# Optimization experiments

Hardware: AMD Instinct MI355X
Metric: run time of the kernel (lower is better)

Reference implementation:

```python
import jax, jax.numpy as jnp
import numpy as np

B, T, HID = 2, 2048, 2048
NH = 8
D = HID // NH  # head_dim = 256 (expand_ratio=1 so input_dim == hidden_size)
EPS_RMS = 1e-8   # RMSNorm inside BitLinear
EPS_LN = 1e-5    # layernorm_eps for g_norm


def _rms(x, w, eps):
    # weighted RMSNorm over last dim
    return x * jax.lax.rsqrt(jnp.mean(x * x, axis=-1, keepdims=True) + eps) * w


def _act_quant(x):
    # per-token 8-bit fake quant with straight-through estimator
    s = 127.0 / jnp.clip(jnp.max(jnp.abs(x), axis=-1, keepdims=True), 1e-5)
    q = jnp.clip(jnp.round(x * s), -128, 127) / s
    return x + jax.lax.stop_gradient(q - x)


def _weight_quant(w):
    # ternary weight quantization (BitNet b1.58) with STE
    s = 1.0 / jnp.clip(jnp.mean(jnp.abs(w)), 1e-5)
    q = jnp.clip(jnp.round(w * s), -1, 1) / s
    return w + jax.lax.stop_gradient(q - w)


def _bitlinear(x, w, norm_w):
    # FusedBitLinear: RMSNorm -> activation quant -> ternary-weight linear
    xq = _act_quant(_rms(x, norm_w, EPS_RMS))
    return jnp.einsum('btk,ok->bto', xq, _weight_quant(w))


def setup_inputs() -> dict:
    key = jax.random.key(0)
    ks = jax.random.split(key, 5)
    std = 2 ** (-2.5) * np.sqrt(2.0 / (HID + HID))  # xavier_uniform-ish std with gain 2^-2.5
    return {
        'hidden_states': jax.random.normal(ks[0], (B, T, HID), dtype=jnp.float32),
        'w_i': jax.random.normal(ks[1], (HID, HID), dtype=jnp.float32) * std,
        'w_f': jax.random.normal(ks[2], (HID, HID), dtype=jnp.float32) * std,
        'w_g': jax.random.normal(ks[3], (HID, HID), dtype=jnp.float32) * std,
        'w_o': jax.random.normal(ks[4], (HID, HID), dtype=jnp.float32) * std,
        'n_i': jnp.ones((HID,), jnp.float32),
        'n_f': jnp.ones((HID,), jnp.float32),
        'n_g': jnp.ones((HID,), jnp.float32),
        'n_o': jnp.ones((HID,), jnp.float32),
        'gn_w': jnp.ones((HID,), jnp.float32),
    }


def reference(hidden_states, w_i, w_f, w_g, w_o, n_i, n_f, n_g, n_o, gn_w):
    hs = hidden_states
    i = _bitlinear(hs, w_i, n_i)                      # [B,T,HID]
    f = jax.nn.sigmoid(_bitlinear(hs, w_f, n_f))      # forget gate
    # swiglu(i, 1 - f) = silu(i) * (1 - f)
    i = i * jax.nn.sigmoid(i) * (1.0 - f)

    # b l (h d) -> t b h d for scan
    def to_tbhd(x):
        return x.reshape(B, T, NH, D).transpose(1, 0, 2, 3)

    i_t, f_t = to_tbhd(i), to_tbhd(f)

    def step(h, ft_it):
        ft, it = ft_it
        h = ft * h + it
        return h, h

    h0 = jnp.zeros((B, NH, D), dtype=i.dtype)
    _, o = jax.lax.scan(step, h0, (f_t, i_t))         # [T,B,NH,D]
    o = o.transpose(1, 0, 2, 3).reshape(B, T, HID)     # b l (h d)

    # g_norm(g_proj(hs), o): rmsnorm(g) * o * sigmoid(o)
    g = _bitlinear(hs, w_g, n_g)
    o = _rms(g, gn_w, EPS_LN) * o * jax.nn.sigmoid(o)
    return _bitlinear(o, w_o, n_o)
```

## Files before the change

kernel.cpp:

```cpp
#include <hip/hip_runtime.h>
#include <math.h>

#define HID 2048
#define TOKENS 4096
#define TT 2048
#define NCH 4096
#define NC 32
#define CL 64
#define WELEM 4194304

typedef unsigned short u16;
typedef signed char i8;
typedef int i32x4 __attribute__((ext_vector_type(4)));

__device__ inline float sigm(float x) { return 1.0f / (1.0f + expf(-x)); }
__device__ inline u16 f2bf_rn(float v) {
  unsigned b = __float_as_uint(v);
  unsigned r = b + 0x7FFFu + ((b >> 16) & 1u);
  return (u16)(r >> 16);
}
__device__ inline float bf2f(u16 h) {
  return __uint_as_float((unsigned)h << 16);
}

__device__ inline float wred_sum(float v) {
#pragma unroll
  for (int o = 32; o > 0; o >>= 1) v += __shfl_down(v, o);
  return v;
}
__device__ inline float wred_max(float v) {
#pragma unroll
  for (int o = 32; o > 0; o >>= 1) v = fmaxf(v, __shfl_down(v, o));
  return v;
}
__device__ inline double wred_sumd(double v) {
#pragma unroll
  for (int o = 32; o > 0; o >>= 1) v += __shfl_down(v, o);
  return v;
}

__device__ __forceinline__ void gl_lds16(const void* g, void* l) {
  __builtin_amdgcn_global_load_lds(
      (__attribute__((address_space(1))) void*)(void*)g,
      (__attribute__((address_space(3))) void*)l, 16, 0, 0);
}

__device__ __forceinline__ int pack8(const int* qi) {
  return (qi[0] & 255) | ((qi[1] & 255) << 8) | ((qi[2] & 255) << 16)
       | ((qi[3] & 255) << 24);
}

__global__ __launch_bounds__(256) void absmean_kernel(
    const float* __restrict__ w0, const float* __restrict__ w1,
    const float* __restrict__ w2, const float* __restrict__ w3,
    double* __restrict__ wsum) {
  int widx = blockIdx.x >> 9;
  int blk = blockIdx.x & 511;
  const float* w = widx == 0 ? w0 : widx == 1 ? w1 : widx == 2 ? w2 : w3;
  size_t base = (size_t)blk * 8192;
  double acc = 0.0;
#pragma unroll
  for (int r = 0; r < 8; ++r) {
    float4 v = *(const float4*)&w[base + (size_t)(r * 256 + threadIdx.x) * 4];
    acc += (double)fabsf(v.x) + (double)fabsf(v.y) + (double)fabsf(v.z) +
           (double)fabsf(v.w);
  }
  acc = wred_sumd(acc);
  __shared__ double sh[4];
  int tid = threadIdx.x;
  if ((tid & 63) == 0) sh[tid >> 6] = acc;
  __syncthreads();
  if (tid == 0) atomicAdd(&wsum[widx], (sh[0] + sh[1]) + (sh[2] + sh[3]));
}

__global__ __launch_bounds__(256) void prep_kernel(
    const float* __restrict__ w0, const float* __restrict__ w1,
    const float* __restrict__ w2, const float* __restrict__ w3,
    const double* __restrict__ wsum, i8* __restrict__ q0, i8* __restrict__ q1,
    i8* __restrict__ q2, i8* __restrict__ q3, const float* __restrict__ X,
    const float* __restrict__ nw0, const float* __restrict__ nw1,
    const float* __restrict__ nw2, i8* __restrict__ Xq0, i8* __restrict__ Xq1,
    i8* __restrict__ Xq2, float* __restrict__ inv0, float* __restrict__ inv1,
    float* __restrict__ inv2) {
  if (blockIdx.x < 8192) {
    int sel = blockIdx.x >> 11;
    int blk = blockIdx.x & 2047;
    const float* w = sel == 0 ? w0 : sel == 1 ? w1 : sel == 2 ? w2 : w3;
    i8* wq = sel == 0 ? q0 : sel == 1 ? q1 : sel == 2 ? q2 : q3;
    int widx = sel == 0 ? 1 : sel == 1 ? 0 : sel;
    double mean = wsum[widx] * (1.0 / (double)WELEM);
    float s = (float)(1.0 / fmax(mean, 1e-5));
    size_t base = (size_t)blk * 2048 + (size_t)threadIdx.x * 8;
    float4 va = *(const float4*)&w[base];
    float4 vb = *(const float4*)&w[base + 4];
    float vv[8] = {va.x, va.y, va.z, va.w, vb.x, vb.y, vb.z, vb.w};
    int qi[8];
#pragma unroll
    for (int j = 0; j < 8; ++j) {
      float q1v = rintf(vv[j] * s);
      q1v = fminf(fmaxf(q1v, -1.0f), 1.0f);
      qi[j] = (int)q1v;
    }
    *(int2*)&wq[base] = make_int2(pack8(qi), pack8(qi + 4));
    return;
  }
  int tok = blockIdx.x - 8192;
  int tid = threadIdx.x;
  const float* xrow = X + (size_t)tok * HID;
  int c0 = tid * 8;
  float x[8];
  *(float4*)&x[0] = *(const float4*)&xrow[c0];
  *(float4*)&x[4] = *(const float4*)&xrow[c0 + 4];
  float ss = 0.0f;
#pragma unroll
  for (int j = 0; j < 8; ++j) ss += x[j] * x[j];
  __shared__ float sh[4];
  float v = wred_sum(ss);
  if ((tid & 63) == 0) sh[tid >> 6] = v;
  __syncthreads();
  float tot = (sh[0] + sh[1]) + (sh[2] + sh[3]);
  float rstd = (float)(1.0 / sqrt((double)(tot * (1.0f / HID)) + 1e-8));
#pragma unroll
  for (int pass = 0; pass < 3; ++pass) {
    const float* nw = pass == 0 ? nw0 : pass == 1 ? nw1 : nw2;
    i8* Xq = pass == 0 ? Xq0 : pass == 1 ? Xq1 : Xq2;
    float* inv_s = pass == 0 ? inv0 : pass == 1 ? inv1 : inv2;
    float y[8];
    float amax = 0.0f;
#pragma unroll
    for (int j = 0; j < 8; ++j) {
      y[j] = x[j] * rstd * nw[c0 + j];
      amax = fmaxf(amax, fabsf(y[j]));
    }
    __syncthreads();
    float vv = wred_max(amax);
    if ((tid & 63) == 0) sh[tid >> 6] = vv;
    __syncthreads();
    float am = fmaxf(fmaxf(fmaxf(sh[0], sh[1]), fmaxf(sh[2], sh[3])), 1e-5f);
    float s = 127.0f / am;
    int qi[8];
#pragma unroll
    for (int j = 0; j < 8; ++j) {
      float qq = rintf(y[j] * s);
      qq = fminf(fmaxf(qq, -128.0f), 127.0f);
      qi[j] = (int)qq;
    }
    *(int2*)&Xq[(size_t)tok * HID + c0] = make_int2(pack8(qi), pack8(qi + 4));
    if (tid == 0) inv_s[tok] = am * (1.0f / 127.0f);
  }
}

template <int NSEG, bool F32OUT>
__global__ __launch_bounds__(512) void gemm8_kernel(
    const i8* __restrict__ A0, const i8* __restrict__ A1,
    const i8* __restrict__ A2, const i8* __restrict__ W0,
    const i8* __restrict__ W1, const i8* __restrict__ W2,
    const float* __restrict__ inv0, const float* __restrict__ inv1,
    const float* __restrict__ inv2, const double* __restrict__ wsum,
    int widx0, int widx1, int widx2, void* __restrict__ O0,
    void* __restrict__ O1, void* __restrict__ O2) {
  const int tid = threadIdx.x;
  const int cpx = gridDim.x >> 3;
  const int lid = blockIdx.x;
  const int swz = (lid & 7) * cpx + (lid >> 3);
  const int seg = NSEG == 1 ? 0 : (swz >> 9);
  const int idx = swz & 511;
  const int n0 = (idx & 15) * 128;
  const int m0 = (idx >> 4) * 128;

  const i8* Aq = seg == 0 ? A0 : seg == 1 ? A1 : A2;
  const i8* Wq = seg == 0 ? W0 : seg == 1 ? W1 : W2;
  const float* inv_s = seg == 0 ? inv0 : seg == 1 ? inv1 : inv2;
  void* Out = seg == 0 ? O0 : seg == 1 ? O1 : O2;
  const int widx = seg == 0 ? widx0 : seg == 1 ? widx1 : widx2;

  __shared__ __align__(16) i8 As[2][16384];
  __shared__ __align__(16) i8 Bs[2][16384];
  float wscale = (float)fmax(wsum[widx] * (1.0 / (double)WELEM), 1e-5);

  const int wave = tid >> 6, lane = tid & 63;
  const int wm = wave >> 2;
  const int wn = wave & 3;
  const int lrow = lane & 15;
  const int ksel = lane >> 4;
  const int rsw = lrow & 7;
  const int srow8 = lane >> 3;
  const int scol = ((lane & 7) ^ srow8) << 4;

  const i8* Ab = Aq + (size_t)m0 * HID;
  const i8* Wb = Wq + (size_t)n0 * HID;

  i32x4 acc[4][2];
#pragma unroll
  for (int i = 0; i < 4; ++i)
#pragma unroll
    for (int j = 0; j < 2; ++j)
#pragma unroll
      for (int r = 0; r < 4; ++r) acc[i][j][r] = 0;

#define STAGE(buf, k0)                                                      \
  {                                                                         \
    _Pragma("unroll") for (int c = 0; c < 2; ++c) {                         \
      int chunk = wave * 2 + c;                                             \
      int row = chunk * 8 + srow8;                                          \
      gl_lds16(&Ab[(size_t)row * HID + (k0) + scol], &As[buf][chunk * 1024]); \
      gl_lds16(&Wb[(size_t)row * HID + (k0) + scol], &Bs[buf][chunk * 1024]); \
    }                                                                       \
  }

  const int NT = HID / 128;
  STAGE(0, 0)
  __syncthreads();
  int cur = 0;
  for (int kt = 0; kt < NT; ++kt) {
    if (kt + 1 < NT) STAGE(cur ^ 1, (kt + 1) * 128)
    i32x4 af[4][2], bfr[2][2];
#pragma unroll
    for (int i = 0; i < 4; ++i) {
      int ra = wm * 64 + i * 16 + lrow;
#pragma unroll
      for (int kk = 0; kk < 2; ++kk) {
        int phys = ((kk << 2) | ksel) ^ rsw;
        af[i][kk] = *(const i32x4*)&As[cur][ra * 128 + phys * 16];
      }
    }
#pragma unroll
    for (int j = 0; j < 2; ++j) {
      int rb = wn * 32 + j * 16 + lrow;
#pragma unroll
      for (int kk = 0; kk < 2; ++kk) {
        int phys = ((kk << 2) | ksel) ^ rsw;
        bfr[j][kk] = *(const i32x4*)&Bs[cur][rb * 128 + phys * 16];
      }
    }
    __builtin_amdgcn_s_setprio(1);
#pragma unroll
    for (int kk = 0; kk < 2; ++kk)
#pragma unroll
      for (int i = 0; i < 4; ++i)
#pragma unroll
        for (int j = 0; j < 2; ++j)
          acc[i][j] = __builtin_amdgcn_mfma_i32_16x16x64_i8(
              af[i][kk], bfr[j][kk], acc[i][j], 0, 0, 0);
    __builtin_amdgcn_s_setprio(0);
    __syncthreads();
    cur ^= 1;
  }
#undef STAGE

#pragma unroll
  for (int i = 0; i < 4; ++i) {
    int rbase = m0 + wm * 64 + i * 16 + (lane >> 4) * 4;
#pragma unroll
    for (int j = 0; j < 2; ++j) {
      int col = n0 + wn * 32 + j * 16 + lrow;
#pragma unroll
      for (int r = 0; r < 4; ++r) {
        int row = rbase + r;
        float v = (float)acc[i][j][r] * inv_s[row] * wscale;
        float rr;
        if (NSEG == 3)
          rr = seg == 0 ? sigm(v) : seg == 1 ? v * sigm(v) : v;
        else
          rr = v;
        size_t oidx = (size_t)row * HID + col;
        if (F32OUT)
          ((float*)Out)[oidx] = rr;
        else
          ((u16*)Out)[oidx] = f2bf_rn(rr);
      }
    }
  }
}

__global__ __launch_bounds__(256) void scan1_kernel(
    const u16* __restrict__ F, u16* __restrict__ IO, float* __restrict__ P,
    float* __restrict__ H) {
  int c = blockIdx.x * 256 + threadIdx.x;
  int q = blockIdx.y;
  size_t base =
      (size_t)(c >> 11) * TT * HID + (c & 2047) + (size_t)q * CL * HID;
  float h = 0.0f, p = 1.0f;
#pragma unroll 4
  for (int t = 0; t < CL; ++t) {
    size_t idx = base + (size_t)t * HID;
    float f = bf2f(F[idx]);
    float iv = bf2f(IO[idx]);
    h = fmaf(f, h, iv - iv * f);
    p *= f;
    IO[idx] = f2bf_rn(h);
  }
  P[q * NCH + c] = p;
  H[q * NCH + c] = h;
}

__global__ __launch_bounds__(256) void scan23_kernel(
    const u16* __restrict__ F, const float* __restrict__ P,
    const float* __restrict__ H, u16* __restrict__ IO) {
  int c = blockIdx.x * 256 + threadIdx.x;
  int q = blockIdx.y + 1;
  float carry = 0.0f;
  for (int qq = 0; qq < q; ++qq)
    carry = fmaf(P[qq * NCH + c], carry, H[qq * NCH + c]);
  if (carry == 0.0f) return;
  size_t base =
      (size_t)(c >> 11) * TT * HID + (c & 2047) + (size_t)q * CL * HID;
  float p = 1.0f;
#pragma unroll 4
  for (int t = 0; t < CL; ++t) {
    size_t idx = base + (size_t)t * HID;
    p *= bf2f(F[idx]);
    IO[idx] = f2bf_rn(fmaf(p, carry, bf2f(IO[idx])));
  }
}

__global__ __launch_bounds__(256) void combine_quant_kernel(
    const u16* __restrict__ G, const float* __restrict__ gnw,
    const u16* __restrict__ O, const float* __restrict__ nw,
    i8* __restrict__ Xq, float* __restrict__ inv_s) {
  int tok = blockIdx.x;
  int tid = threadIdx.x;
  int c0 = tid * 8;
  const u16* grow = G + (size_t)tok * HID;
  const u16* orow = O + (size_t)tok * HID;
  ushort4 ga = *(const ushort4*)&grow[c0];
  ushort4 gb = *(const ushort4*)&grow[c0 + 4];
  ushort4 oa = *(const ushort4*)&orow[c0];
  ushort4 ob = *(const ushort4*)&orow[c0 + 4];
  float g[8] = {bf2f(ga.x), bf2f(ga.y), bf2f(ga.z), bf2f(ga.w),
                bf2f(gb.x), bf2f(gb.y), bf2f(gb.z), bf2f(gb.w)};
  float o[8] = {bf2f(oa.x), bf2f(oa.y), bf2f(oa.z), bf2f(oa.w),
                bf2f(ob.x), bf2f(ob.y), bf2f(ob.z), bf2f(ob.w)};
  __shared__ float sh[4];
  float ss = 0.0f;
#pragma unroll
  for (int j = 0; j < 8; ++j) ss += g[j] * g[j];
  float v = wred_sum(ss);
  if ((tid & 63) == 0) sh[tid >> 6] = v;
  __syncthreads();
  float tot = (sh[0] + sh[1]) + (sh[2] + sh[3]);
  float rstd_g = (float)(1.0 / sqrt((double)(tot * (1.0f / HID)) + 1e-5));
  float on[8];
  float ss2 = 0.0f;
#pragma unroll
  for (int j = 0; j < 8; ++j) {
    on[j] = g[j] * rstd_g * gnw[c0 + j] * o[j] * sigm(o[j]);
    ss2 += on[j] * on[j];
  }
  __syncthreads();
  v = wred_sum(ss2);
  if ((tid & 63) == 0) sh[tid >> 6] = v;
  __syncthreads();
  float tot2 = (sh[0] + sh[1]) + (sh[2] + sh[3]);
  float rstd_o = (float)(1.0 / sqrt((double)(tot2 * (1.0f / HID)) + 1e-8));
  float y[8];
  float amax = 0.0f;
#pragma unroll
  for (int j = 0; j < 8; ++j) {
    y[j] = on[j] * rstd_o * nw[c0 + j];
    amax = fmaxf(amax, fabsf(y[j]));
  }
  __syncthreads();
  v = wred_max(amax);
  if ((tid & 63) == 0) sh[tid >> 6] = v;
  __syncthreads();
  float am = fmaxf(fmaxf(fmaxf(sh[0], sh[1]), fmaxf(sh[2], sh[3])), 1e-5f);
  float s = 127.0f / am;
  int qi[8];
#pragma unroll
  for (int j = 0; j < 8; ++j) {
    float qq = rintf(y[j] * s);
    qq = fminf(fmaxf(qq, -128.0f), 127.0f);
    qi[j] = (int)qq;
  }
  *(int2*)&Xq[(size_t)tok * HID + c0] = make_int2(pack8(qi), pack8(qi + 4));
  if (tid == 0) inv_s[tok] = am * (1.0f / 127.0f);
}

extern "C" void kernel_launch(void* const* d_in, const int* in_sizes, int n_in,
                              void* d_out, int out_size, void* d_ws,
                              size_t ws_size, hipStream_t stream) {
  const float* hs = (const float*)d_in[0];
  const float* w_i = (const float*)d_in[1];
  const float* w_f = (const float*)d_in[2];
  const float* w_g = (const float*)d_in[3];
  const float* w_o = (const float*)d_in[4];
  const float* n_i = (const float*)d_in[5];
  const float* n_f = (const float*)d_in[6];
  const float* n_g = (const float*)d_in[7];
  const float* n_o = (const float*)d_in[8];
  const float* gn_w = (const float*)d_in[9];
  float* Out = (float*)d_out;

  char* ws = (char*)d_ws;
  i8* WQ0 = (i8*)ws;
  i8* WQ1 = (i8*)(ws + 4194304);
  i8* WQ2 = (i8*)(ws + 8388608);
  i8* WQ3 = (i8*)(ws + 12582912);
  i8* XQ0 = (i8*)(ws + 16777216);
  i8* XQ1 = (i8*)(ws + 25165824);
  i8* XQ2 = (i8*)(ws + 33554432);
  u16* F = (u16*)(ws + 41943040);
  u16* OB = (u16*)(ws + 58720256);
  u16* G = (u16*)(ws + 75497472);
  float* invs0 = (float*)(ws + 92274688);
  float* invs1 = (float*)(ws + 92291072);
  float* invs2 = (float*)(ws + 92307456);
  double* wsum = (double*)(ws + 92323840);
  float* scanP = (float*)(ws + 92324864);
  float* scanH = (float*)(ws + 92849152);

  hipMemsetAsync(wsum, 0, 4 * sizeof(double), stream);
  absmean_kernel<<<2048, 256, 0, stream>>>(w_i, w_f, w_g, w_o, wsum);

  prep_kernel<<<12288, 256, 0, stream>>>(w_f, w_i, w_g, w_o, wsum, WQ0, WQ1,
                                         WQ2, WQ3, hs, n_f, n_i, n_g, XQ0,
                                         XQ1, XQ2, invs0, invs1, invs2);

  gemm8_kernel<3, false><<<1536, 512, 0, stream>>>(
      XQ0, XQ1, XQ2, WQ0, WQ1, WQ2, invs0, invs1, invs2, wsum, 1, 0, 2, F, OB,
      G);

  scan1_kernel<<<dim3(NCH / 256, NC), 256, 0, stream>>>(F, OB, scanP, scanH);
  scan23_kernel<<<dim3(NCH / 256, NC - 1), 256, 0, stream>>>(F, scanP, scanH,
                                                             OB);

  combine_quant_kernel<<<TOKENS, 256, 0, stream>>>(G, gn_w, OB, n_o, XQ0,
                                                   invs0);

  gemm8_kernel<1, true><<<512, 512, 0, stream>>>(
      XQ0, XQ0, XQ0, WQ3, WQ3, WQ3, invs0, invs0, invs0, wsum, 3, 3, 3, Out,
      Out, Out);
}
```

Measured before the change: 198.1 us.

## Switch int8 GEMM to 32x32x32 MFMA and vectorize scan kernels two channels per thread

The int8 GEMM's per-wave tile now uses 32x32x32 i8 MFMA instructions with 16-element accumulators instead of eight 16x16x64 ones. The LDS fragment loads and the epilogue row/column mapping are rewritten to match. This should cut MFMA issue count and LDS reads per k-step. Separately, both scan kernels now process two adjacent channels per thread with 32-bit packed bf16 loads and stores, halving the grid. The gain is wider memory accesses, at the cost of less parallelism and a coarser early-exit test.

Measured after the change: 217.7 us. +9.9%, slower.

```diff
diff --git a/kernel.cpp b/kernel.cpp
--- a/kernel.cpp
+++ b/kernel.cpp
@@ -10,8 +10,10 @@
 #define WELEM 4194304
 
 typedef unsigned short u16;
+typedef unsigned int u32;
 typedef signed char i8;
 typedef int i32x4 __attribute__((ext_vector_type(4)));
+typedef int i32x16 __attribute__((ext_vector_type(16)));
 
 __device__ inline float sigm(float x) { return 1.0f / (1.0f + expf(-x)); }
 __device__ inline u16 f2bf_rn(float v) {
@@ -181,22 +183,20 @@
   const int wave = tid >> 6, lane = tid & 63;
   const int wm = wave >> 2;
   const int wn = wave & 3;
-  const int lrow = lane & 15;
-  const int ksel = lane >> 4;
-  const int rsw = lrow & 7;
+  const int l31 = lane & 31;
+  const int khalf = lane >> 5;
+  const int rkey = l31 & 7;
   const int srow8 = lane >> 3;
   const int scol = ((lane & 7) ^ srow8) << 4;
 
   const i8* Ab = Aq + (size_t)m0 * HID;
   const i8* Wb = Wq + (size_t)n0 * HID;
 
-  i32x4 acc[4][2];
-#pragma unroll
-  for (int i = 0; i < 4; ++i)
-#pragma unroll
-    for (int j = 0; j < 2; ++j)
-#pragma unroll
-      for (int r = 0; r < 4; ++r) acc[i][j][r] = 0;
+  i32x16 acc2[2];
+#pragma unroll
+  for (int mi = 0; mi < 2; ++mi)
+#pragma unroll
+    for (int r = 0; r < 16; ++r) acc2[mi][r] = 0;
 
 #define STAGE(buf, k0)                                                      \
   {                                                                         \
@@ -214,34 +214,22 @@
   int cur = 0;
   for (int kt = 0; kt < NT; ++kt) {
     if (kt + 1 < NT) STAGE(cur ^ 1, (kt + 1) * 128)
-    i32x4 af[4][2], bfr[2][2];
-#pragma unroll
-    for (int i = 0; i < 4; ++i) {
-      int ra = wm * 64 + i * 16 + lrow;
-#pragma unroll
-      for (int kk = 0; kk < 2; ++kk) {
-        int phys = ((kk << 2) | ksel) ^ rsw;
-        af[i][kk] = *(const i32x4*)&As[cur][ra * 128 + phys * 16];
-      }
-    }
-#pragma unroll
-    for (int j = 0; j < 2; ++j) {
-      int rb = wn * 32 + j * 16 + lrow;
-#pragma unroll
-      for (int kk = 0; kk < 2; ++kk) {
-        int phys = ((kk << 2) | ksel) ^ rsw;
-        bfr[j][kk] = *(const i32x4*)&Bs[cur][rb * 128 + phys * 16];
-      }
+    i32x4 af[2][4], bf[4];
+#pragma unroll
+    for (int s = 0; s < 4; ++s) {
+      int pco = ((s * 2 + khalf) ^ rkey) * 16;
+      af[0][s] = *(const i32x4*)&As[cur][(wm * 64 + l31) * 128 + pco];
+      af[1][s] = *(const i32x4*)&As[cur][(wm * 64 + 32 + l31) * 128 + pco];
+      bf[s] = *(const i32x4*)&Bs[cur][(wn * 32 + l31) * 128 + pco];
     }
     __builtin_amdgcn_s_setprio(1);
 #pragma unroll
-    for (int kk = 0; kk < 2; ++kk)
-#pragma unroll
-      for (int i = 0; i < 4; ++i)
-#pragma unroll
-        for (int j = 0; j < 2; ++j)
-          acc[i][j] = __builtin_amdgcn_mfma_i32_16x16x64_i8(
-              af[i][kk], bfr[j][kk], acc[i][j], 0, 0, 0);
+    for (int s = 0; s < 4; ++s) {
+      acc2[0] = __builtin_amdgcn_mfma_i32_32x32x32_i8(af[0][s], bf[s],
+                                                      acc2[0], 0, 0, 0);
+      acc2[1] = __builtin_amdgcn_mfma_i32_32x32x32_i8(af[1][s], bf[s],
+                                                      acc2[1], 0, 0, 0);
+    }
     __builtin_amdgcn_s_setprio(0);
     __syncthreads();
     cur ^= 1;
@@ -249,26 +237,22 @@
 #undef STAGE
 
 #pragma unroll
-  for (int i = 0; i < 4; ++i) {
-    int rbase = m0 + wm * 64 + i * 16 + (lane >> 4) * 4;
-#pragma unroll
-    for (int j = 0; j < 2; ++j) {
-      int col = n0 + wn * 32 + j * 16 + lrow;
-#pragma unroll
-      for (int r = 0; r < 4; ++r) {
-        int row = rbase + r;
-        float v = (float)acc[i][j][r] * inv_s[row] * wscale;
-        float rr;
-        if (NSEG == 3)
-          rr = seg == 0 ? sigm(v) : seg == 1 ? v * sigm(v) : v;
-        else
-          rr = v;
-        size_t oidx = (size_t)row * HID + col;
-        if (F32OUT)
-          ((float*)Out)[oidx] = rr;
-        else
-          ((u16*)Out)[oidx] = f2bf_rn(rr);
-      }
+  for (int mi = 0; mi < 2; ++mi) {
+#pragma unroll
+    for (int r = 0; r < 16; ++r) {
+      int row = m0 + wm * 64 + mi * 32 + (r & 3) + 8 * (r >> 2) + 4 * khalf;
+      int col = n0 + wn * 32 + l31;
+      float v = (float)acc2[mi][r] * inv_s[row] * wscale;
+      float rr;
+      if (NSEG == 3)
+        rr = seg == 0 ? sigm(v) : seg == 1 ? v * sigm(v) : v;
+      else
+        rr = v;
+      size_t oidx = (size_t)row * HID + col;
+      if (F32OUT)
+        ((float*)Out)[oidx] = rr;
+      else
+        ((u16*)Out)[oidx] = f2bf_rn(rr);
     }
   }
 }
@@ -276,41 +260,56 @@
 __global__ __launch_bounds__(256) void scan1_kernel(
     const u16* __restrict__ F, u16* __restrict__ IO, float* __restrict__ P,
     float* __restrict__ H) {
-  int c = blockIdx.x * 256 + threadIdx.x;
+  int g = blockIdx.x * 256 + threadIdx.x;
+  int c0 = g * 2;
   int q = blockIdx.y;
   size_t base =
-      (size_t)(c >> 11) * TT * HID + (c & 2047) + (size_t)q * CL * HID;
-  float h = 0.0f, p = 1.0f;
+      (size_t)(c0 >> 11) * TT * HID + (c0 & 2047) + (size_t)q * CL * HID;
+  float h0 = 0.0f, h1 = 0.0f, p0 = 1.0f, p1 = 1.0f;
 #pragma unroll 4
   for (int t = 0; t < CL; ++t) {
     size_t idx = base + (size_t)t * HID;
-    float f = bf2f(F[idx]);
-    float iv = bf2f(IO[idx]);
-    h = fmaf(f, h, iv - iv * f);
-    p *= f;
-    IO[idx] = f2bf_rn(h);
-  }
-  P[q * NCH + c] = p;
-  H[q * NCH + c] = h;
+    u32 fw = *(const u32*)&F[idx];
+    u32 iw = *(const u32*)&IO[idx];
+    float f0 = bf2f((u16)fw), f1 = bf2f((u16)(fw >> 16));
+    float i0 = bf2f((u16)iw), i1 = bf2f((u16)(iw >> 16));
+    h0 = fmaf(f0, h0, i0 - i0 * f0);
+    h1 = fmaf(f1, h1, i1 - i1 * f1);
+    p0 *= f0;
+    p1 *= f1;
+    *(u32*)&IO[idx] = (u32)f2bf_rn(h0) | ((u32)f2bf_rn(h1) << 16);
+  }
+  *(float2*)&P[q * NCH + c0] = make_float2(p0, p1);
+  *(float2*)&H[q * NCH + c0] = make_float2(h0, h1);
 }
 
 __global__ __launch_bounds__(256) void scan23_kernel(
     const u16* __restrict__ F, const float* __restrict__ P,
     const float* __restrict__ H, u16* __restrict__ IO) {
-  int c = blockIdx.x * 256 + threadIdx.x;
+  int g = blockIdx.x * 256 + threadIdx.x;
+  int c0 = g * 2;
   int q = blockIdx.y + 1;
-  float carry = 0.0f;
-  for (int qq = 0; qq < q; ++qq)
-    carry = fmaf(P[qq * NCH + c], carry, H[qq * NCH + c]);
-  if (carry == 0.0f) return;
+  float cy0 = 0.0f, cy1 = 0.0f;
+  for (int qq = 0; qq < q; ++qq) {
+    float2 pq = *(const float2*)&P[qq * NCH + c0];
+    float2 hq = *(const float2*)&H[qq * NCH + c0];
+    cy0 = fmaf(pq.x, cy0, hq.x);
+    cy1 = fmaf(pq.y, cy1, hq.y);
+  }
+  if (cy0 == 0.0f && cy1 == 0.0f) return;
   size_t base =
-      (size_t)(c >> 11) * TT * HID + (c & 2047) + (size_t)q * CL * HID;
-  float p = 1.0f;
+      (size_t)(c0 >> 11) * TT * HID + (c0 & 2047) + (size_t)q * CL * HID;
+  float p0 = 1.0f, p1 = 1.0f;
 #pragma unroll 4
   for (int t = 0; t < CL; ++t) {
     size_t idx = base + (size_t)t * HID;
-    p *= bf2f(F[idx]);
-    IO[idx] = f2bf_rn(fmaf(p, carry, bf2f(IO[idx])));
+    u32 fw = *(const u32*)&F[idx];
+    u32 iw = *(const u32*)&IO[idx];
+    p0 *= bf2f((u16)fw);
+    p1 *= bf2f((u16)(fw >> 16));
+    float o0 = fmaf(p0, cy0, bf2f((u16)iw));
+    float o1 = fmaf(p1, cy1, bf2f((u16)(iw >> 16)));
+    *(u32*)&IO[idx] = (u32)f2bf_rn(o0) | ((u32)f2bf_rn(o1) << 16);
   }
 }
 
@@ -421,8 +420,8 @@
       XQ0, XQ1, XQ2, WQ0, WQ1, WQ2, invs0, invs1, invs2, wsum, 1, 0, 2, F, OB,
       G);
 
-  scan1_kernel<<<dim3(NCH / 256, NC), 256, 0, stream>>>(F, OB, scanP, scanH);
-  scan23_kernel<<<dim3(NCH / 256, NC - 1), 256, 0, stream>>>(F, scanP, scanH,
+  scan1_kernel<<<dim3(NCH / 512, NC), 256, 0, stream>>>(F, OB, scanP, scanH);
+  scan23_kernel<<<dim3(NCH / 512, NC - 1), 256, 0, stream>>>(F, scanP, scanH,
                                                              OB);
 
   combine_quant_kernel<<<TOKENS, 256, 0, stream>>>(G, gn_w, OB, n_o, XQ0,
```
